# Kernel tuning notes

Measured on AMD Instinct MI355X. Metric: run time of the kernel, lower is better.

Reference implementation:

```python
import jax, jax.numpy as jnp
import numpy as np

NSAMPLE = 1024   # FPS centroids S
NGROUP = 32      # neighbors per ball K
RADIUS = 0.2


def _sqdist(a, b):
    # a: [B,S,3], b: [B,N,3] -> [B,S,N] squared euclidean distances
    return (jnp.sum(a * a, -1)[:, :, None]
            + jnp.sum(b * b, -1)[:, None, :]
            - 2.0 * jnp.einsum('bsc,bnc->bsn', a, b))


def farthest_point_sample(xyz, npoint):
    # xyz: [B,N,3] -> indices [B,npoint]. Deterministic start at index 0
    # (torch version randomizes the first centroid).
    B, N, _ = xyz.shape

    def step(carry, _):
        distance, farthest = carry
        centroid = jnp.take_along_axis(xyz, farthest[:, None, None], axis=1)  # [B,1,3]
        d = jnp.sum((xyz - centroid) ** 2, -1)                                 # [B,N]
        distance = jnp.minimum(distance, d)
        new_far = jnp.argmax(distance, -1).astype(jnp.int32)
        return (distance, new_far), farthest

    init = (jnp.full((B, N), 1e10, xyz.dtype), jnp.zeros((B,), jnp.int32))
    _, cents = jax.lax.scan(step, init, None, length=npoint)  # [npoint,B]
    return cents.T  # [B,npoint]


def query_ball_point(radius, nsample, xyz, new_xyz):
    # xyz: [B,N,3], new_xyz: [B,S,3] -> int idx [B,S,nsample]
    B, N, _ = xyz.shape
    sqr = _sqdist(new_xyz, xyz)                       # [B,S,N]
    idx = jnp.broadcast_to(jnp.arange(N, dtype=jnp.int32), sqr.shape)
    idx = jnp.where(sqr > radius * radius, N, idx)    # invalid -> sentinel N
    idx = jnp.sort(idx, axis=-1)[:, :, :nsample]      # smallest valid indices first
    first = idx[:, :, :1]
    idx = jnp.where(idx == N, first, idx)             # pad with first neighbor
    return idx.astype(jnp.int32)


def _gather_points(points, idx):
    # points: [B,N,C], idx: [B,S,K] -> [B,S,K,C]
    return jax.vmap(lambda p, i: p[i])(points, idx)


def setup_inputs() -> dict:
    key = jax.random.key(0)
    ks = jax.random.split(key, 8)
    B, N, D = 16, 8192, 64
    xyz = jax.random.uniform(ks[0], (B, N, 3), dtype=jnp.float32)
    points_fea = jax.random.normal(ks[1], (B, N, D), dtype=jnp.float32)
    s = 0.05
    W1 = jax.random.normal(ks[2], (67, 64), dtype=jnp.float32) * s
    b1 = jnp.zeros((64,), jnp.float32)
    W2 = jax.random.normal(ks[3], (64, 128), dtype=jnp.float32) * s
    b2 = jnp.zeros((128,), jnp.float32)
    W3 = jax.random.normal(ks[4], (128, 256), dtype=jnp.float32) * s
    b3 = jnp.zeros((256,), jnp.float32)
    return {"xyz": xyz, "points_fea": points_fea, "W1": W1, "b1": b1,
            "W2": W2, "b2": b2, "W3": W3, "b3": b3}


def reference(xyz, points_fea, W1, b1, W2, b2, W3, b3):
    # --- sample_and_group (fps + ball query) ---
    fps_idx = farthest_point_sample(xyz, NSAMPLE)                       # [B,S]
    sampled_xyz = jnp.take_along_axis(xyz, fps_idx[..., None], axis=1)  # [B,S,3]
    grouped_idx = query_ball_point(RADIUS, NGROUP, xyz, sampled_xyz)    # [B,S,K]
    grouped_xyz = _gather_points(xyz, grouped_idx)                      # [B,S,K,3]
    rel = grouped_xyz - sampled_xyz[:, :, None, :]
    grouped_fea = _gather_points(points_fea, grouped_idx)               # [B,S,K,D]
    feats = jnp.concatenate([rel, grouped_fea], axis=-1)                # [B,S,K,3+D]
    # --- per-point MLP (Linear+ReLU x3) ---
    h = jax.nn.relu(feats @ W1 + b1)
    h = jax.nn.relu(h @ W2 + b2)
    h = jax.nn.relu(h @ W3 + b3)                                        # [B,S,K,256]
    # --- max-pool over neighbors ---
    out = jnp.max(h, axis=2)                                            # [B,S,256]
    return sampled_xyz, out
```

## Files before the change

kernel.cpp:

```cpp
#include <hip/hip_runtime.h>
#include <hip/hip_bf16.h>

#define N_PTS 8192
#define NSAMP 1024
#define NGRP  32

typedef __attribute__((ext_vector_type(8))) short bf16x8;
typedef __attribute__((ext_vector_type(4))) float f32x4;

static __device__ inline unsigned short f2bf(float f) {
  __hip_bfloat16 h = __float2bfloat16(f);
  return __builtin_bit_cast(unsigned short, h);
}

#define DPP_MAXSTEP(r, ctrl)                                                  \
  r = fmaxf(r, __int_as_float(__builtin_amdgcn_update_dpp(                    \
          __float_as_int(r), __float_as_int(r), (ctrl), 0xf, 0xf, false)))

__global__
__attribute__((amdgpu_flat_work_group_size(512, 512)))
__attribute__((amdgpu_waves_per_eu(2, 2)))
void fps_kernel(
    const float* __restrict__ xyz, float* __restrict__ out_sampled)
{
  #pragma clang fp contract(off)
  const int b = blockIdx.x;
  const int t = threadIdx.x;
  const float* bx = xyz + (size_t)b * N_PTS * 3;

  float px[16], py[16], pz[16], dist[16];
  {
    const float4* src = (const float4*)(bx + t * 48);
    float4 v0 = src[0], v1 = src[1], v2 = src[2];
    float4 v3 = src[3], v4 = src[4], v5 = src[5];
    float4 v6 = src[6], v7 = src[7], v8 = src[8];
    float4 v9 = src[9], v10 = src[10], v11 = src[11];
    px[ 0]=v0.x; py[ 0]=v0.y; pz[ 0]=v0.z;
    px[ 1]=v0.w; py[ 1]=v1.x; pz[ 1]=v1.y;
    px[ 2]=v1.z; py[ 2]=v1.w; pz[ 2]=v2.x;
    px[ 3]=v2.y; py[ 3]=v2.z; pz[ 3]=v2.w;
    px[ 4]=v3.x; py[ 4]=v3.y; pz[ 4]=v3.z;
    px[ 5]=v3.w; py[ 5]=v4.x; pz[ 5]=v4.y;
    px[ 6]=v4.z; py[ 6]=v4.w; pz[ 6]=v5.x;
    px[ 7]=v5.y; py[ 7]=v5.z; pz[ 7]=v5.w;
    px[ 8]=v6.x; py[ 8]=v6.y; pz[ 8]=v6.z;
    px[ 9]=v6.w; py[ 9]=v7.x; pz[ 9]=v7.y;
    px[10]=v7.z; py[10]=v7.w; pz[10]=v8.x;
    px[11]=v8.y; py[11]=v8.z; pz[11]=v8.w;
    px[12]=v9.x; py[12]=v9.y; pz[12]=v9.z;
    px[13]=v9.w; py[13]=v10.x; pz[13]=v10.y;
    px[14]=v10.z; py[14]=v10.w; pz[14]=v11.x;
    px[15]=v11.y; py[15]=v11.z; pz[15]=v11.w;
  }
  #pragma unroll
  for (int r = 0; r < 16; ++r) dist[r] = 10000000000.0f;

  __shared__ uint2 part[2][8];
  __shared__ float out_lds[NSAMP * 3];

  const int lane = t & 63;
  const int wv   = t >> 6;

  float cx = bx[0], cy = bx[1], cz = bx[2];

  for (int it = 0; it < NSAMP; ++it) {
    if (t == 0) {
      out_lds[it * 3 + 0] = cx;
      out_lds[it * 3 + 1] = cy;
      out_lds[it * 3 + 2] = cz;
    }

    float bv = -1.0f;
    #pragma unroll
    for (int r = 0; r < 16; ++r) {
      float dx = px[r] - cx;
      float dy = py[r] - cy;
      float dz = pz[r] - cz;
      float d  = fmaf(dz, dz, fmaf(dy, dy, dx * dx));
      float nd = fminf(dist[r], d);
      dist[r] = nd;
      bv = fmaxf(bv, nd);
    }
    int bi = t * 16 + 15;
    #pragma unroll
    for (int r = 14; r >= 0; --r) bi = (dist[r] == bv) ? (t * 16 + r) : bi;

    float rmax = bv;
    DPP_MAXSTEP(rmax, 0x111);
    DPP_MAXSTEP(rmax, 0x112);
    DPP_MAXSTEP(rmax, 0x114);
    DPP_MAXSTEP(rmax, 0x118);
    DPP_MAXSTEP(rmax, 0x142);
    DPP_MAXSTEP(rmax, 0x143);
    float vmax = __int_as_float(
        __builtin_amdgcn_readlane(__float_as_int(rmax), 63));

    unsigned long long m = __ballot(bv == vmax);
    int L = __ffsll((long long)m) - 1;
    int widx = __builtin_amdgcn_readlane(bi, L);

    const int slot = it & 1;
    if (lane == 0) part[slot][wv] = make_uint2(__float_as_uint(vmax), (unsigned)widx);
    __syncthreads();

    const uint4* pp = (const uint4*)&part[slot][0];
    uint4 p0 = pp[0], p1 = pp[1], p2 = pp[2], p3 = pp[3];
    float v = __uint_as_float(p0.x); unsigned f = p0.y;
    float w1v = __uint_as_float(p0.z);
    if (w1v > v) { v = w1v; f = p0.w; }
    float w2v = __uint_as_float(p1.x);
    if (w2v > v) { v = w2v; f = p1.y; }
    float w3v = __uint_as_float(p1.z);
    if (w3v > v) { v = w3v; f = p1.w; }
    float w4v = __uint_as_float(p2.x);
    if (w4v > v) { v = w4v; f = p2.y; }
    float w5v = __uint_as_float(p2.z);
    if (w5v > v) { v = w5v; f = p2.w; }
    float w6v = __uint_as_float(p3.x);
    if (w6v > v) { v = w6v; f = p3.y; }
    float w7v = __uint_as_float(p3.z);
    if (w7v > v) { v = w7v; f = p3.w; }

    cx = bx[f * 3 + 0];
    cy = bx[f * 3 + 1];
    cz = bx[f * 3 + 2];
  }

  __syncthreads();
  float* ob = out_sampled + (size_t)b * NSAMP * 3;
  for (int i = t; i < NSAMP * 3; i += 512) ob[i] = out_lds[i];
}

__global__ __launch_bounds__(256) void ball_kernel(
    const float* __restrict__ xyz, const float* __restrict__ sampled,
    int* __restrict__ gidx)
{
  #pragma clang fp contract(off)
  const float R2 = (float)(0.2 * 0.2);
  int gt = blockIdx.x * 256 + threadIdx.x;
  int w = gt >> 6;
  int lane = gt & 63;
  const int b = w >> 10;
  const float* cp = sampled + (size_t)w * 3;
  float cx = cp[0], cy = cp[1], cz = cp[2];
  float na = ((cx * cx) + (cy * cy)) + (cz * cz);
  const float* bx = xyz + (size_t)b * N_PTS * 3;
  int* out = gidx + (size_t)w * NGRP;

  int cnt = 0;
  int first = 0;
  for (int base = 0; base < N_PTS && cnt < NGRP; base += 64) {
    int p = base + lane;
    float x = bx[p * 3 + 0];
    float y = bx[p * 3 + 1];
    float z = bx[p * 3 + 2];
    float nb  = ((x * x) + (y * y)) + (z * z);
    float dot = fmaf(cz, z, fmaf(cy, y, cx * x));
    float sq  = (na + nb) - (2.0f * dot);
    bool inr = !(sq > R2);
    unsigned long long m = __ballot(inr);
    if (cnt == 0 && m != 0ull) first = base + (__ffsll(m) - 1);
    int before = __popcll(m & ((1ull << lane) - 1ull));
    int pos = cnt + before;
    if (inr && pos < NGRP) out[pos] = p;
    cnt += __popcll(m);
  }
  if (cnt < NGRP) {
    int q = cnt + lane;
    if (q < NGRP) out[q] = first;
  }
}

__global__ __launch_bounds__(256) void prep_w_kernel(
    const float* __restrict__ W1, const float* __restrict__ W2,
    const float* __restrict__ W3, unsigned short* __restrict__ wf1,
    unsigned short* __restrict__ wf2, unsigned short* __restrict__ wf3)
{
  int tid = blockIdx.x * 256 + threadIdx.x;
  int rec = tid >> 6, lane = tid & 63;
  if (rec >= 92) return;
  const float* W; unsigned short* dst; int N, K, ksteps, rl;
  if (rec < 12)      { W = W1; dst = wf1; N = 64;  K = 67;  ksteps = 3; rl = rec; }
  else if (rec < 28) { W = W2; dst = wf2; N = 128; K = 64;  ksteps = 2; rl = rec - 12; }
  else               { W = W3; dst = wf3; N = 256; K = 128; ksteps = 4; rl = rec - 28; }
  int nt = rl / ksteps, ks = rl - nt * ksteps;
  int n  = nt * 16 + (lane & 15);
  int kb = ks * 32 + (lane >> 4) * 8;
  unsigned short v[8] __attribute__((aligned(16)));
  #pragma unroll
  for (int j = 0; j < 8; ++j) {
    int k = kb + j;
    v[j] = f2bf((k < K) ? W[k * N + n] : 0.0f);
  }
  *(uint4*)(dst + ((size_t)rl * 64 + lane) * 8) = *(const uint4*)v;
}

__global__ __launch_bounds__(256, 4) void mlp_mfma_kernel(
    const float* __restrict__ xyz, const float* __restrict__ fea,
    const float* __restrict__ sampled, const int* __restrict__ gidx,
    const unsigned short* __restrict__ wf1, const unsigned short* __restrict__ wf2,
    const unsigned short* __restrict__ wf3, const float* __restrict__ b1,
    const float* __restrict__ b2, const float* __restrict__ b3,
    float* __restrict__ out)
{
  __shared__ __align__(16) unsigned short fT[32][104];
  __shared__ __align__(16) unsigned short h1[32][72];
  __shared__ __align__(16) unsigned short h2[32][136];
  __shared__ float pmax[8][256];
  __shared__ int   sidx[32];
  __shared__ float sc[4];

  const int bs = blockIdx.x;
  const int b  = bs >> 10;
  const int t  = threadIdx.x;
  const int w    = t >> 6;
  const int lane = t & 63;
  const int quad = lane >> 4;
  const int ncol = lane & 15;

  if (t < 32) sidx[t] = gidx[(size_t)bs * 32 + t];
  if (t < 3)  sc[t] = sampled[(size_t)bs * 3 + t];
  __syncthreads();

  {
    const int pt = t >> 3, c0 = t & 7;
    const int p = sidx[pt];
    const float* xp = xyz + ((size_t)b * N_PTS + p) * 3;
    const float* fp = fea + ((size_t)b * N_PTS + p) * 64;
    for (int c = c0; c < 96; c += 8) {
      float v = (c < 3) ? (xp[c] - sc[c]) : (c < 67 ? fp[c - 3] : 0.0f);
      fT[pt][c] = f2bf(v);
    }
  }
  __syncthreads();

  #pragma unroll
  for (int q2 = 0; q2 < 2; ++q2) {
    const int tid = w * 2 + q2, mt = tid & 1, nt = tid >> 1;
    float bb = b1[nt * 16 + ncol];
    f32x4 acc = {bb, bb, bb, bb};
    #pragma unroll
    for (int ks = 0; ks < 3; ++ks) {
      bf16x8 a = *(const bf16x8*)&fT[mt * 16 + ncol][ks * 32 + quad * 8];
      bf16x8 bf = *(const bf16x8*)(wf1 + ((size_t)(nt * 3 + ks) * 64 + lane) * 8);
      acc = __builtin_amdgcn_mfma_f32_16x16x32_bf16(a, bf, acc, 0, 0, 0);
    }
    #pragma unroll
    for (int r = 0; r < 4; ++r)
      h1[mt * 16 + quad * 4 + r][nt * 16 + ncol] = f2bf(fmaxf(acc[r], 0.0f));
  }
  __syncthreads();

  #pragma unroll
  for (int q2 = 0; q2 < 4; ++q2) {
    const int tid = w * 4 + q2, mt = tid & 1, nt = tid >> 1;
    float bb = b2[nt * 16 + ncol];
    f32x4 acc = {bb, bb, bb, bb};
    #pragma unroll
    for (int ks = 0; ks < 2; ++ks) {
      bf16x8 a = *(const bf16x8*)&h1[mt * 16 + ncol][ks * 32 + quad * 8];
      bf16x8 bf = *(const bf16x8*)(wf2 + ((size_t)(nt * 2 + ks) * 64 + lane) * 8);
      acc = __builtin_amdgcn_mfma_f32_16x16x32_bf16(a, bf, acc, 0, 0, 0);
    }
    #pragma unroll
    for (int r = 0; r < 4; ++r)
      h2[mt * 16 + quad * 4 + r][nt * 16 + ncol] = f2bf(fmaxf(acc[r], 0.0f));
  }
  __syncthreads();

  #pragma unroll
  for (int q2 = 0; q2 < 8; ++q2) {
    const int tid = w * 8 + q2, mt = tid & 1, nt = tid >> 1;
    float bb = b3[nt * 16 + ncol];
    f32x4 acc = {bb, bb, bb, bb};
    #pragma unroll
    for (int ks = 0; ks < 4; ++ks) {
      bf16x8 a = *(const bf16x8*)&h2[mt * 16 + ncol][ks * 32 + quad * 8];
      bf16x8 bf = *(const bf16x8*)(wf3 + ((size_t)(nt * 4 + ks) * 64 + lane) * 8);
      acc = __builtin_amdgcn_mfma_f32_16x16x32_bf16(a, bf, acc, 0, 0, 0);
    }
    float mx = fmaxf(fmaxf(acc[0], acc[1]), fmaxf(acc[2], acc[3]));
    pmax[mt * 4 + quad][nt * 16 + ncol] = mx;
  }
  __syncthreads();

  {
    float v = pmax[0][t];
    #pragma unroll
    for (int s = 1; s < 8; ++s) v = fmaxf(v, pmax[s][t]);
    out[(size_t)bs * 256 + t] = fmaxf(v, 0.0f);
  }
}

extern "C" void kernel_launch(void* const* d_in, const int* in_sizes, int n_in,
                              void* d_out, int out_size, void* d_ws, size_t ws_size,
                              hipStream_t stream) {
  const float* xyz = (const float*)d_in[0];
  const float* fea = (const float*)d_in[1];
  const float* W1  = (const float*)d_in[2];
  const float* b1  = (const float*)d_in[3];
  const float* W2  = (const float*)d_in[4];
  const float* b2  = (const float*)d_in[5];
  const float* W3  = (const float*)d_in[6];
  const float* b3  = (const float*)d_in[7];

  float* outp    = (float*)d_out;
  float* sampled = outp;
  float* mlp_out = outp + 16 * 1024 * 3;
  int*   gidx    = (int*)d_ws;
  unsigned short* wf1 = (unsigned short*)((char*)d_ws + (2u << 20));
  unsigned short* wf2 = wf1 + (size_t)12 * 64 * 8;
  unsigned short* wf3 = wf2 + (size_t)16 * 64 * 8;

  fps_kernel<<<16, 512, 0, stream>>>(xyz, sampled);
  prep_w_kernel<<<23, 256, 0, stream>>>(W1, W2, W3, wf1, wf2, wf3);
  ball_kernel<<<4096, 256, 0, stream>>>(xyz, sampled, gidx);
  mlp_mfma_kernel<<<16384, 256, 0, stream>>>(xyz, fea, sampled, gidx,
                                             wf1, wf2, wf3, b1, b2, b3, mlp_out);
}
```

Measured before the change: 1.096 ms.

## Process two batches per FPS block to interleave independent reduction chains

The farthest point sampling kernel now handles two batch elements per 512-thread block, running their distance updates, DPP reductions, ballots and barriers interleaved. The aim is to hide the latency of the serial per-iteration reduction and barrier chain behind a second independent chain, and to halve the number of barriers per sample. In exchange, register use doubles, which may cause spills under the two-waves-per-EU bound, and only 8 blocks run, so fewer CUs are used for FPS.

```diff
diff --git a/kernel.cpp b/kernel.cpp
--- a/kernel.cpp
+++ b/kernel.cpp
@@ -16,6 +16,45 @@
 #define DPP_MAXSTEP(r, ctrl)                                                  \
   r = fmaxf(r, __int_as_float(__builtin_amdgcn_update_dpp(                    \
           __float_as_int(r), __float_as_int(r), (ctrl), 0xf, 0xf, false)))
+
+#define FINAL8(P, V, F) do {                                                  \
+    const uint4* pp_ = (const uint4*)&(P)[0];                                 \
+    uint4 p0_ = pp_[0], p1_ = pp_[1], p2_ = pp_[2], p3_ = pp_[3];             \
+    V = __uint_as_float(p0_.x); F = p0_.y;                                    \
+    float q_;                                                                 \
+    q_ = __uint_as_float(p0_.z); if (q_ > V) { V = q_; F = p0_.w; }           \
+    q_ = __uint_as_float(p1_.x); if (q_ > V) { V = q_; F = p1_.y; }           \
+    q_ = __uint_as_float(p1_.z); if (q_ > V) { V = q_; F = p1_.w; }           \
+    q_ = __uint_as_float(p2_.x); if (q_ > V) { V = q_; F = p2_.y; }           \
+    q_ = __uint_as_float(p2_.z); if (q_ > V) { V = q_; F = p2_.w; }           \
+    q_ = __uint_as_float(p3_.x); if (q_ > V) { V = q_; F = p3_.y; }           \
+    q_ = __uint_as_float(p3_.z); if (q_ > V) { V = q_; F = p3_.w; }           \
+  } while (0)
+
+static __device__ inline void load16(const float* __restrict__ bx, int t,
+                                     float px[16], float py[16], float pz[16]) {
+  const float4* src = (const float4*)(bx + t * 48);
+  float4 v0 = src[0], v1 = src[1], v2 = src[2];
+  float4 v3 = src[3], v4 = src[4], v5 = src[5];
+  float4 v6 = src[6], v7 = src[7], v8 = src[8];
+  float4 v9 = src[9], v10 = src[10], v11 = src[11];
+  px[ 0]=v0.x; py[ 0]=v0.y; pz[ 0]=v0.z;
+  px[ 1]=v0.w; py[ 1]=v1.x; pz[ 1]=v1.y;
+  px[ 2]=v1.z; py[ 2]=v1.w; pz[ 2]=v2.x;
+  px[ 3]=v2.y; py[ 3]=v2.z; pz[ 3]=v2.w;
+  px[ 4]=v3.x; py[ 4]=v3.y; pz[ 4]=v3.z;
+  px[ 5]=v3.w; py[ 5]=v4.x; pz[ 5]=v4.y;
+  px[ 6]=v4.z; py[ 6]=v4.w; pz[ 6]=v5.x;
+  px[ 7]=v5.y; py[ 7]=v5.z; pz[ 7]=v5.w;
+  px[ 8]=v6.x; py[ 8]=v6.y; pz[ 8]=v6.z;
+  px[ 9]=v6.w; py[ 9]=v7.x; pz[ 9]=v7.y;
+  px[10]=v7.z; py[10]=v7.w; pz[10]=v8.x;
+  px[11]=v8.y; py[11]=v8.z; pz[11]=v8.w;
+  px[12]=v9.x; py[12]=v9.y; pz[12]=v9.z;
+  px[13]=v9.w; py[13]=v10.x; pz[13]=v10.y;
+  px[14]=v10.z; py[14]=v10.w; pz[14]=v11.x;
+  px[15]=v11.y; py[15]=v11.z; pz[15]=v11.w;
+}
 
 __global__
 __attribute__((amdgpu_flat_work_group_size(512, 512)))
@@ -24,111 +63,98 @@
     const float* __restrict__ xyz, float* __restrict__ out_sampled)
 {
   #pragma clang fp contract(off)
-  const int b = blockIdx.x;
-  const int t = threadIdx.x;
-  const float* bx = xyz + (size_t)b * N_PTS * 3;
-
-  float px[16], py[16], pz[16], dist[16];
-  {
-    const float4* src = (const float4*)(bx + t * 48);
-    float4 v0 = src[0], v1 = src[1], v2 = src[2];
-    float4 v3 = src[3], v4 = src[4], v5 = src[5];
-    float4 v6 = src[6], v7 = src[7], v8 = src[8];
-    float4 v9 = src[9], v10 = src[10], v11 = src[11];
-    px[ 0]=v0.x; py[ 0]=v0.y; pz[ 0]=v0.z;
-    px[ 1]=v0.w; py[ 1]=v1.x; pz[ 1]=v1.y;
-    px[ 2]=v1.z; py[ 2]=v1.w; pz[ 2]=v2.x;
-    px[ 3]=v2.y; py[ 3]=v2.z; pz[ 3]=v2.w;
-    px[ 4]=v3.x; py[ 4]=v3.y; pz[ 4]=v3.z;
-    px[ 5]=v3.w; py[ 5]=v4.x; pz[ 5]=v4.y;
-    px[ 6]=v4.z; py[ 6]=v4.w; pz[ 6]=v5.x;
-    px[ 7]=v5.y; py[ 7]=v5.z; pz[ 7]=v5.w;
-    px[ 8]=v6.x; py[ 8]=v6.y; pz[ 8]=v6.z;
-    px[ 9]=v6.w; py[ 9]=v7.x; pz[ 9]=v7.y;
-    px[10]=v7.z; py[10]=v7.w; pz[10]=v8.x;
-    px[11]=v8.y; py[11]=v8.z; pz[11]=v8.w;
-    px[12]=v9.x; py[12]=v9.y; pz[12]=v9.z;
-    px[13]=v9.w; py[13]=v10.x; pz[13]=v10.y;
-    px[14]=v10.z; py[14]=v10.w; pz[14]=v11.x;
-    px[15]=v11.y; py[15]=v11.z; pz[15]=v11.w;
-  }
-  #pragma unroll
-  for (int r = 0; r < 16; ++r) dist[r] = 10000000000.0f;
-
-  __shared__ uint2 part[2][8];
-  __shared__ float out_lds[NSAMP * 3];
+  const int b0 = blockIdx.x * 2;
+  const int t  = threadIdx.x;
+  const float* bxA = xyz + (size_t)b0 * N_PTS * 3;
+  const float* bxB = xyz + (size_t)(b0 + 1) * N_PTS * 3;
+
+  float pxA[16], pyA[16], pzA[16], dsA[16];
+  float pxB[16], pyB[16], pzB[16], dsB[16];
+  load16(bxA, t, pxA, pyA, pzA);
+  load16(bxB, t, pxB, pyB, pzB);
+  #pragma unroll
+  for (int r = 0; r < 16; ++r) { dsA[r] = 10000000000.0f; dsB[r] = 10000000000.0f; }
+
+  __shared__ __align__(16) uint2 part[2][2][8];
+  __shared__ float out_lds[2][NSAMP * 3];
 
   const int lane = t & 63;
   const int wv   = t >> 6;
 
-  float cx = bx[0], cy = bx[1], cz = bx[2];
+  float cxA = bxA[0], cyA = bxA[1], czA = bxA[2];
+  float cxB = bxB[0], cyB = bxB[1], czB = bxB[2];
 
   for (int it = 0; it < NSAMP; ++it) {
     if (t == 0) {
-      out_lds[it * 3 + 0] = cx;
-      out_lds[it * 3 + 1] = cy;
-      out_lds[it * 3 + 2] = cz;
-    }
-
-    float bv = -1.0f;
+      out_lds[0][it * 3 + 0] = cxA;
+      out_lds[0][it * 3 + 1] = cyA;
+      out_lds[0][it * 3 + 2] = czA;
+      out_lds[1][it * 3 + 0] = cxB;
+      out_lds[1][it * 3 + 1] = cyB;
+      out_lds[1][it * 3 + 2] = czB;
+    }
+
+    float bvA = -1.0f, bvB = -1.0f;
     #pragma unroll
     for (int r = 0; r < 16; ++r) {
-      float dx = px[r] - cx;
-      float dy = py[r] - cy;
-      float dz = pz[r] - cz;
-      float d  = fmaf(dz, dz, fmaf(dy, dy, dx * dx));
-      float nd = fminf(dist[r], d);
-      dist[r] = nd;
-      bv = fmaxf(bv, nd);
-    }
-    int bi = t * 16 + 15;
-    #pragma unroll
-    for (int r = 14; r >= 0; --r) bi = (dist[r] == bv) ? (t * 16 + r) : bi;
-
-    float rmax = bv;
-    DPP_MAXSTEP(rmax, 0x111);
-    DPP_MAXSTEP(rmax, 0x112);
-    DPP_MAXSTEP(rmax, 0x114);
-    DPP_MAXSTEP(rmax, 0x118);
-    DPP_MAXSTEP(rmax, 0x142);
-    DPP_MAXSTEP(rmax, 0x143);
-    float vmax = __int_as_float(
-        __builtin_amdgcn_readlane(__float_as_int(rmax), 63));
-
-    unsigned long long m = __ballot(bv == vmax);
-    int L = __ffsll((long long)m) - 1;
-    int widx = __builtin_amdgcn_readlane(bi, L);
+      float dxA = pxA[r] - cxA, dyA = pyA[r] - cyA, dzA = pzA[r] - czA;
+      float dxB = pxB[r] - cxB, dyB = pyB[r] - cyB, dzB = pzB[r] - czB;
+      float dA  = fmaf(dzA, dzA, fmaf(dyA, dyA, dxA * dxA));
+      float dB  = fmaf(dzB, dzB, fmaf(dyB, dyB, dxB * dxB));
+      float ndA = fminf(dsA[r], dA);
+      float ndB = fminf(dsB[r], dB);
+      dsA[r] = ndA;            dsB[r] = ndB;
+      bvA = fmaxf(bvA, ndA);   bvB = fmaxf(bvB, ndB);
+    }
+    int biA = t * 16 + 15, biB = t * 16 + 15;
+    #pragma unroll
+    for (int r = 14; r >= 0; --r) {
+      biA = (dsA[r] == bvA) ? (t * 16 + r) : biA;
+      biB = (dsB[r] == bvB) ? (t * 16 + r) : biB;
+    }
+
+    float rmA = bvA, rmB = bvB;
+    DPP_MAXSTEP(rmA, 0x111); DPP_MAXSTEP(rmB, 0x111);
+    DPP_MAXSTEP(rmA, 0x112); DPP_MAXSTEP(rmB, 0x112);
+    DPP_MAXSTEP(rmA, 0x114); DPP_MAXSTEP(rmB, 0x114);
+    DPP_MAXSTEP(rmA, 0x118); DPP_MAXSTEP(rmB, 0x118);
+    DPP_MAXSTEP(rmA, 0x142); DPP_MAXSTEP(rmB, 0x142);
+    DPP_MAXSTEP(rmA, 0x143); DPP_MAXSTEP(rmB, 0x143);
+    float vmA = __int_as_float(
+        __builtin_amdgcn_readlane(__float_as_int(rmA), 63));
+    float vmB = __int_as_float(
+        __builtin_amdgcn_readlane(__float_as_int(rmB), 63));
+
+    unsigned long long mA = __ballot(bvA == vmA);
+    unsigned long long mB = __ballot(bvB == vmB);
+    int LA = __ffsll((long long)mA) - 1;
+    int LB = __ffsll((long long)mB) - 1;
+    int wiA = __builtin_amdgcn_readlane(biA, LA);
+    int wiB = __builtin_amdgcn_readlane(biB, LB);
 
     const int slot = it & 1;
-    if (lane == 0) part[slot][wv] = make_uint2(__float_as_uint(vmax), (unsigned)widx);
+    if (lane == 0) {
+      part[slot][0][wv] = make_uint2(__float_as_uint(vmA), (unsigned)wiA);
+      part[slot][1][wv] = make_uint2(__float_as_uint(vmB), (unsigned)wiB);
+    }
     __syncthreads();
 
-    const uint4* pp = (const uint4*)&part[slot][0];
-    uint4 p0 = pp[0], p1 = pp[1], p2 = pp[2], p3 = pp[3];
-    float v = __uint_as_float(p0.x); unsigned f = p0.y;
-    float w1v = __uint_as_float(p0.z);
-    if (w1v > v) { v = w1v; f = p0.w; }
-    float w2v = __uint_as_float(p1.x);
-    if (w2v > v) { v = w2v; f = p1.y; }
-    float w3v = __uint_as_float(p1.z);
-    if (w3v > v) { v = w3v; f = p1.w; }
-    float w4v = __uint_as_float(p2.x);
-    if (w4v > v) { v = w4v; f = p2.y; }
-    float w5v = __uint_as_float(p2.z);
-    if (w5v > v) { v = w5v; f = p2.w; }
-    float w6v = __uint_as_float(p3.x);
-    if (w6v > v) { v = w6v; f = p3.y; }
-    float w7v = __uint_as_float(p3.z);
-    if (w7v > v) { v = w7v; f = p3.w; }
-
-    cx = bx[f * 3 + 0];
-    cy = bx[f * 3 + 1];
-    cz = bx[f * 3 + 2];
-  }
-
-  __syncthreads();
-  float* ob = out_sampled + (size_t)b * NSAMP * 3;
-  for (int i = t; i < NSAMP * 3; i += 512) ob[i] = out_lds[i];
+    float vA; unsigned fA;
+    float vB; unsigned fB;
+    FINAL8(part[slot][0], vA, fA);
+    FINAL8(part[slot][1], vB, fB);
+
+    cxA = bxA[fA * 3 + 0]; cyA = bxA[fA * 3 + 1]; czA = bxA[fA * 3 + 2];
+    cxB = bxB[fB * 3 + 0]; cyB = bxB[fB * 3 + 1]; czB = bxB[fB * 3 + 2];
+  }
+
+  __syncthreads();
+  float* obA = out_sampled + (size_t)b0 * NSAMP * 3;
+  float* obB = obA + NSAMP * 3;
+  for (int i = t; i < NSAMP * 3; i += 512) {
+    obA[i] = out_lds[0][i];
+    obB[i] = out_lds[1][i];
+  }
 }
 
 __global__ __launch_bounds__(256) void ball_kernel(
@@ -312,7 +338,7 @@
   unsigned short* wf2 = wf1 + (size_t)12 * 64 * 8;
   unsigned short* wf3 = wf2 + (size_t)16 * 64 * 8;
 
-  fps_kernel<<<16, 512, 0, stream>>>(xyz, sampled);
+  fps_kernel<<<8, 512, 0, stream>>>(xyz, sampled);
   prep_w_kernel<<<23, 256, 0, stream>>>(W1, W2, W3, wf1, wf2, wf3);
   ball_kernel<<<4096, 256, 0, stream>>>(xyz, sampled, gidx);
   mlp_mfma_kernel<<<16384, 256, 0, stream>>>(xyz, fea, sampled, gidx,
```

Result: slower. 1.800 ms (+64.1%).

## Pack FPS distance math into float2 ops and stage points in LDS

Applied to the files above, without the earlier changes.

The FPS kernel now holds point coordinates and running distances as float2 pairs so the compiler can emit packed FP32 instructions (v_pk_*), roughly halving the per-iteration ALU instruction count. The whole batch's xyz (96KB) is also copied into LDS once, so each iteration reads the next centroid from LDS instead of global memory, taking global latency off the serial loop-carried dependency. The large LDS allocation limits the kernel to one block per CU, which matters little since there are only 16 blocks. Packed math must keep the exact fma ordering to preserve bit-identical argmax ties.

```diff
diff --git a/kernel.cpp b/kernel.cpp
--- a/kernel.cpp
+++ b/kernel.cpp
@@ -7,6 +7,7 @@
 
 typedef __attribute__((ext_vector_type(8))) short bf16x8;
 typedef __attribute__((ext_vector_type(4))) float f32x4;
+typedef __attribute__((ext_vector_type(2))) float f32x2;
 
 static __device__ inline unsigned short f2bf(float f) {
   __hip_bfloat16 h = __float2bfloat16(f);
@@ -16,6 +17,45 @@
 #define DPP_MAXSTEP(r, ctrl)                                                  \
   r = fmaxf(r, __int_as_float(__builtin_amdgcn_update_dpp(                    \
           __float_as_int(r), __float_as_int(r), (ctrl), 0xf, 0xf, false)))
+
+#define FINAL8(P, V, F) do {                                                  \
+    const uint4* pp_ = (const uint4*)&(P)[0];                                 \
+    uint4 p0_ = pp_[0], p1_ = pp_[1], p2_ = pp_[2], p3_ = pp_[3];             \
+    V = __uint_as_float(p0_.x); F = p0_.y;                                    \
+    float q_;                                                                 \
+    q_ = __uint_as_float(p0_.z); if (q_ > V) { V = q_; F = p0_.w; }           \
+    q_ = __uint_as_float(p1_.x); if (q_ > V) { V = q_; F = p1_.y; }           \
+    q_ = __uint_as_float(p1_.z); if (q_ > V) { V = q_; F = p1_.w; }           \
+    q_ = __uint_as_float(p2_.x); if (q_ > V) { V = q_; F = p2_.y; }           \
+    q_ = __uint_as_float(p2_.z); if (q_ > V) { V = q_; F = p2_.w; }           \
+    q_ = __uint_as_float(p3_.x); if (q_ > V) { V = q_; F = p3_.y; }           \
+    q_ = __uint_as_float(p3_.z); if (q_ > V) { V = q_; F = p3_.w; }           \
+  } while (0)
+
+static __device__ inline void load16(const float* __restrict__ bx, int t,
+                                     float px[16], float py[16], float pz[16]) {
+  const float4* src = (const float4*)(bx + t * 48);
+  float4 v0 = src[0], v1 = src[1], v2 = src[2];
+  float4 v3 = src[3], v4 = src[4], v5 = src[5];
+  float4 v6 = src[6], v7 = src[7], v8 = src[8];
+  float4 v9 = src[9], v10 = src[10], v11 = src[11];
+  px[ 0]=v0.x; py[ 0]=v0.y; pz[ 0]=v0.z;
+  px[ 1]=v0.w; py[ 1]=v1.x; pz[ 1]=v1.y;
+  px[ 2]=v1.z; py[ 2]=v1.w; pz[ 2]=v2.x;
+  px[ 3]=v2.y; py[ 3]=v2.z; pz[ 3]=v2.w;
+  px[ 4]=v3.x; py[ 4]=v3.y; pz[ 4]=v3.z;
+  px[ 5]=v3.w; py[ 5]=v4.x; pz[ 5]=v4.y;
+  px[ 6]=v4.z; py[ 6]=v4.w; pz[ 6]=v5.x;
+  px[ 7]=v5.y; py[ 7]=v5.z; pz[ 7]=v5.w;
+  px[ 8]=v6.x; py[ 8]=v6.y; pz[ 8]=v6.z;
+  px[ 9]=v6.w; py[ 9]=v7.x; pz[ 9]=v7.y;
+  px[10]=v7.z; py[10]=v7.w; pz[10]=v8.x;
+  px[11]=v8.y; py[11]=v8.z; pz[11]=v8.w;
+  px[12]=v9.x; py[12]=v9.y; pz[12]=v9.z;
+  px[13]=v9.w; py[13]=v10.x; pz[13]=v10.y;
+  px[14]=v10.z; py[14]=v10.w; pz[14]=v11.x;
+  px[15]=v11.y; py[15]=v11.z; pz[15]=v11.w;
+}
 
 __global__
 __attribute__((amdgpu_flat_work_group_size(512, 512)))
@@ -28,35 +68,23 @@
   const int t = threadIdx.x;
   const float* bx = xyz + (size_t)b * N_PTS * 3;
 
-  float px[16], py[16], pz[16], dist[16];
-  {
-    const float4* src = (const float4*)(bx + t * 48);
-    float4 v0 = src[0], v1 = src[1], v2 = src[2];
-    float4 v3 = src[3], v4 = src[4], v5 = src[5];
-    float4 v6 = src[6], v7 = src[7], v8 = src[8];
-    float4 v9 = src[9], v10 = src[10], v11 = src[11];
-    px[ 0]=v0.x; py[ 0]=v0.y; pz[ 0]=v0.z;
-    px[ 1]=v0.w; py[ 1]=v1.x; pz[ 1]=v1.y;
-    px[ 2]=v1.z; py[ 2]=v1.w; pz[ 2]=v2.x;
-    px[ 3]=v2.y; py[ 3]=v2.z; pz[ 3]=v2.w;
-    px[ 4]=v3.x; py[ 4]=v3.y; pz[ 4]=v3.z;
-    px[ 5]=v3.w; py[ 5]=v4.x; pz[ 5]=v4.y;
-    px[ 6]=v4.z; py[ 6]=v4.w; pz[ 6]=v5.x;
-    px[ 7]=v5.y; py[ 7]=v5.z; pz[ 7]=v5.w;
-    px[ 8]=v6.x; py[ 8]=v6.y; pz[ 8]=v6.z;
-    px[ 9]=v6.w; py[ 9]=v7.x; pz[ 9]=v7.y;
-    px[10]=v7.z; py[10]=v7.w; pz[10]=v8.x;
-    px[11]=v8.y; py[11]=v8.z; pz[11]=v8.w;
-    px[12]=v9.x; py[12]=v9.y; pz[12]=v9.z;
-    px[13]=v9.w; py[13]=v10.x; pz[13]=v10.y;
-    px[14]=v10.z; py[14]=v10.w; pz[14]=v11.x;
-    px[15]=v11.y; py[15]=v11.z; pz[15]=v11.w;
-  }
-  #pragma unroll
-  for (int r = 0; r < 16; ++r) dist[r] = 10000000000.0f;
-
-  __shared__ uint2 part[2][8];
+  float px[16], py[16], pz[16];
+  load16(bx, t, px, py, pz);
+
+  f32x2 px2[8], py2[8], pz2[8], ds2[8];
+  #pragma unroll
+  for (int j = 0; j < 8; ++j) {
+    px2[j] = (f32x2){px[2*j], px[2*j+1]};
+    py2[j] = (f32x2){py[2*j], py[2*j+1]};
+    pz2[j] = (f32x2){pz[2*j], pz[2*j+1]};
+    ds2[j] = (f32x2){10000000000.0f, 10000000000.0f};
+  }
+
+  __shared__ float lds_p[N_PTS * 3];
   __shared__ float out_lds[NSAMP * 3];
+  __shared__ __align__(16) uint2 part[2][8];
+
+  for (int i = t; i < N_PTS * 3; i += 512) lds_p[i] = bx[i];
 
   const int lane = t & 63;
   const int wv   = t >> 6;
@@ -70,20 +98,29 @@
       out_lds[it * 3 + 2] = cz;
     }
 
-    float bv = -1.0f;
-    #pragma unroll
-    for (int r = 0; r < 16; ++r) {
-      float dx = px[r] - cx;
-      float dy = py[r] - cy;
-      float dz = pz[r] - cz;
-      float d  = fmaf(dz, dz, fmaf(dy, dy, dx * dx));
-      float nd = fminf(dist[r], d);
-      dist[r] = nd;
-      bv = fmaxf(bv, nd);
-    }
+    const f32x2 c2x = (f32x2){cx, cx};
+    const f32x2 c2y = (f32x2){cy, cy};
+    const f32x2 c2z = (f32x2){cz, cz};
+    f32x2 bv2 = (f32x2){-1.0f, -1.0f};
+    #pragma unroll
+    for (int j = 0; j < 8; ++j) {
+      f32x2 dx = px2[j] - c2x;
+      f32x2 dy = py2[j] - c2y;
+      f32x2 dz = pz2[j] - c2z;
+      f32x2 d  = __builtin_elementwise_fma(
+          dz, dz, __builtin_elementwise_fma(dy, dy, dx * dx));
+      f32x2 nd = __builtin_elementwise_min(ds2[j], d);
+      ds2[j] = nd;
+      bv2 = __builtin_elementwise_max(bv2, nd);
+    }
+    float bv = fmaxf(bv2.x, bv2.y);
+
     int bi = t * 16 + 15;
     #pragma unroll
-    for (int r = 14; r >= 0; --r) bi = (dist[r] == bv) ? (t * 16 + r) : bi;
+    for (int r = 14; r >= 0; --r) {
+      float dr = (r & 1) ? ds2[r >> 1].y : ds2[r >> 1].x;
+      bi = (dr == bv) ? (t * 16 + r) : bi;
+    }
 
     float rmax = bv;
     DPP_MAXSTEP(rmax, 0x111);
@@ -103,27 +140,12 @@
     if (lane == 0) part[slot][wv] = make_uint2(__float_as_uint(vmax), (unsigned)widx);
     __syncthreads();
 
-    const uint4* pp = (const uint4*)&part[slot][0];
-    uint4 p0 = pp[0], p1 = pp[1], p2 = pp[2], p3 = pp[3];
-    float v = __uint_as_float(p0.x); unsigned f = p0.y;
-    float w1v = __uint_as_float(p0.z);
-    if (w1v > v) { v = w1v; f = p0.w; }
-    float w2v = __uint_as_float(p1.x);
-    if (w2v > v) { v = w2v; f = p1.y; }
-    float w3v = __uint_as_float(p1.z);
-    if (w3v > v) { v = w3v; f = p1.w; }
-    float w4v = __uint_as_float(p2.x);
-    if (w4v > v) { v = w4v; f = p2.y; }
-    float w5v = __uint_as_float(p2.z);
-    if (w5v > v) { v = w5v; f = p2.w; }
-    float w6v = __uint_as_float(p3.x);
-    if (w6v > v) { v = w6v; f = p3.y; }
-    float w7v = __uint_as_float(p3.z);
-    if (w7v > v) { v = w7v; f = p3.w; }
-
-    cx = bx[f * 3 + 0];
-    cy = bx[f * 3 + 1];
-    cz = bx[f * 3 + 2];
+    float v; unsigned f;
+    FINAL8(part[slot], v, f);
+
+    cx = lds_p[f * 3 + 0];
+    cy = lds_p[f * 3 + 1];
+    cz = lds_p[f * 3 + 2];
   }
 
   __syncthreads();
```

Result: faster. 1.052 ms (-4.0%).
